# Kernel optimization log

Hardware: AMD Instinct MI355X
Metric: run time of the kernel (lower is better)

The kernel has to match this reference:

```python
import jax, jax.numpy as jnp
import numpy as np

WIN = 16; DIM = 256; HEADS = 8; B = 2; H = 256; W_ = 256
SEL = 0.25; TEMP = 1.0


def _conv(x, w, b, stride=1, pad=1, groups=1):
    y = jax.lax.conv_general_dilated(
        x, w, (stride, stride), [(pad, pad), (pad, pad)],
        dimension_numbers=('NCHW', 'OIHW', 'NCHW'), feature_group_count=groups)
    return y + b[None, :, None, None]


def _rel_pos_index(w):
    coords = np.stack(np.meshgrid(np.arange(w), np.arange(w), indexing='ij'), 0).reshape(2, -1)
    rel = (coords[:, :, None] - coords[:, None, :]).transpose(1, 2, 0) + w - 1
    return jnp.asarray(rel[:, :, 0] * (2 * w - 1) + rel[:, :, 1])


def setup_inputs():
    key = jax.random.key(0)
    ks = jax.random.split(key, 10)
    C, w = DIM, WIN
    p = lambda k, shp, s=0.02: jax.random.normal(k, shp, jnp.float32) * s
    return dict(
        x=jax.random.normal(ks[0], (B, H, W_, C), jnp.float32),
        sd_w1=p(ks[1], (4, C, 3, 3)), sd_b1=jnp.zeros((4,), jnp.float32),
        sd_w2=p(ks[2], (4, 4, w, w)), sd_b2=jnp.zeros((4,), jnp.float32),
        sd_w3=p(ks[3], (4, 4, 3, 3)), sd_b3=jnp.zeros((4,), jnp.float32),
        in_w=p(ks[4], (3 * C, C)), in_b=jnp.zeros((3 * C,), jnp.float32),
        pe_table=p(ks[5], ((2 * w - 1) ** 2, HEADS)),
        out_w=p(ks[6], (C, C)), out_b=jnp.zeros((C,), jnp.float32),
        oc_w=p(ks[7], (C, 1, 3, 3)), oc_b=jnp.zeros((C,), jnp.float32),
    )


def reference(x, sd_w1, sd_b1, sd_w2, sd_b2, sd_w3, sd_b3, in_w, in_b, pe_table, out_w, out_b, oc_w, oc_b):
    w = WIN; C = DIM; nH = HEADS; hd = C // nH
    xc = jnp.transpose(x, (0, 3, 1, 2))  # [B,C,H,W]
    Bn, _, Hh, Ww = xc.shape
    # --- sparse discriminator: per-window scores / gates / offsets ---
    sd = jax.nn.silu(_conv(xc, sd_w1, sd_b1))
    sd = jax.nn.silu(_conv(sd, sd_w2, sd_b2, stride=w, pad=0))
    sd = _conv(sd, sd_w3, sd_b3)                      # [B,4,Hw,Ww]
    scores = sd[:, 0]
    gates = jax.nn.sigmoid(sd[:, 1])
    offsets = jax.nn.sigmoid(sd[:, 2:4])
    Hw, Www = scores.shape[1], scores.shape[2]
    k = int(Hw * Www * SEL)
    # --- top-k window selection (eval: softmax, straight-through to 1) ---
    gs = jax.nn.softmax(scores.reshape(Bn, -1) / TEMP, axis=-1)
    vals, topk = jax.lax.top_k(gs, k)                 # [B,k]
    scores_delta = (jax.lax.stop_gradient(1.0 - vals) + vals).reshape(-1)
    h_idx = (topk // Www).reshape(-1)
    w_idx = (topk % Www).reshape(-1)
    b_idx = jnp.broadcast_to(jnp.arange(Bn)[:, None], (Bn, k)).reshape(-1)
    g = gates[b_idx, h_idx, w_idx]
    hard = (g > 0.5).astype(jnp.float32)
    gates_delta = jax.lax.stop_gradient(hard - g) + g
    # --- learned-offset window coordinates (trunc like .long()) ---
    h_off = (offsets[b_idx, 0, h_idx, w_idx] * w - w / 2.0).astype(jnp.int32)
    w_off = (offsets[b_idx, 1, h_idx, w_idx] * w - w / 2.0).astype(jnp.int32)
    h1 = jnp.clip(h_idx * w + h_off, 0, Hh - w)
    w1 = jnp.clip(w_idx * w + w_off, 0, Ww - w)
    # --- roi_align (aligned=False, 1 sample/bin): bilinear at half-pixel centers ---
    ar = jnp.arange(w, dtype=jnp.float32) + 0.5
    yy = jnp.clip(h1[:, None].astype(jnp.float32) + ar, 0.0, Hh - 1.0)  # [N,w]
    xx = jnp.clip(w1[:, None].astype(jnp.float32) + ar, 0.0, Ww - 1.0)
    y0 = jnp.floor(yy).astype(jnp.int32); ly = yy - y0
    x0 = jnp.floor(xx).astype(jnp.int32); lx = xx - x0
    y1p = jnp.minimum(y0 + 1, Hh - 1); x1p = jnp.minimum(x0 + 1, Ww - 1)
    bI = b_idx[:, None, None]
    gather = lambda ys, xs: xc[bI, :, ys[:, :, None], xs[:, None, :]]  # [N,w,w,C]
    wy1 = ly[:, :, None, None]; wy0 = 1.0 - wy1
    wx1 = lx[:, None, :, None]; wx0 = 1.0 - wx1
    x_before = (wy0 * wx0 * gather(y0, x0) + wy0 * wx1 * gather(y0, x1p)
                + wy1 * wx0 * gather(y1p, x0) + wy1 * wx1 * gather(y1p, x1p))
    N = x_before.shape[0]
    # --- windowed MHA with relative position bias ---
    qkv = x_before.reshape(N, w * w, C) @ in_w.T + in_b
    q, kk, v = jnp.split(qkv, 3, axis=-1)
    heads = lambda t: t.reshape(N, w * w, nH, hd).transpose(0, 2, 1, 3)
    q, kk, v = heads(q), heads(kk), heads(v)
    pe = pe_table[_rel_pos_index(w)].transpose(2, 0, 1)[None]  # [1,nH,w2,w2]
    attn = jax.nn.softmax(jnp.einsum('nhqd,nhkd->nhqk', q, kk) * hd ** (-0.5) + pe, axis=-1)
    o = jnp.einsum('nhqk,nhkd->nhqd', attn, v).transpose(0, 2, 1, 3).reshape(N, w, w, C)
    x_after = o @ out_w.T + out_b
    delta = (x_after - x_before) * (gates_delta * scores_delta)[:, None, None, None]
    delta = delta * hard[:, None, None, None]  # gate-dropped windows contribute nothing
    # --- scatter-reduce 'mean' back into the image ---
    abs_h = h1[:, None] + jnp.arange(w)
    abs_w = w1[:, None] + jnp.arange(w)
    flat = ((b_idx[:, None, None] * Hh + abs_h[:, :, None]) * Ww + abs_w[:, None, :]).reshape(-1)
    sums = jnp.zeros((Bn * Hh * Ww, C), jnp.float32).at[flat].add(delta.reshape(-1, C))
    cnts = jnp.zeros((Bn * Hh * Ww,), jnp.float32).at[flat].add(
        jnp.broadcast_to(hard[:, None, None], (N, w, w)).reshape(-1))
    mean = jnp.where(cnts[:, None] > 0, sums / jnp.maximum(cnts[:, None], 1.0), 0.0)
    xc = xc + mean.reshape(Bn, Hh, Ww, C).transpose(0, 3, 1, 2)
    out = _conv(xc, oc_w, oc_b, groups=C)  # depthwise 3x3
    return jnp.transpose(out, (0, 2, 3, 1))
```

## Files before the change

### kernel.cpp

```cpp
#include <hip/hip_runtime.h>

typedef __attribute__((ext_vector_type(8))) short short8v;
typedef __attribute__((ext_vector_type(4))) float f32x4;

#define DEV __device__ __forceinline__

DEV float sigmoidf_(float x){ return 1.0f/(1.0f+expf(-x)); }
DEV float siluf_(float x){ return x/(1.0f+expf(-x)); }
DEV ushort f2bf(float f){
  union{float f; unsigned u;} a; a.f = f;
  unsigned r = a.u + 0x7fffu + ((a.u >> 16) & 1u);
  return (ushort)(r >> 16);
}


__global__ void k_w36(const float* __restrict__ w1, float* __restrict__ w36){
  int i = blockIdx.x*256 + threadIdx.x;
  if (i < 9216){
    int kk = i % 9, o = (i/9) & 3, c = i / 36;
    w36[i] = w1[(o*256 + c)*9 + kk];
  }
}

__global__ __launch_bounds__(256) void k_c1a(const float* __restrict__ x,
    const float* __restrict__ w36, float* __restrict__ p36){
  int t = threadIdx.x;
  int p0 = blockIdx.x*512 + t;
  const float* xr0 = x + (size_t)p0*256;
  const float* xr1 = xr0 + 65536;
  float acc0[36], acc1[36];
  #pragma unroll
  for (int j=0;j<36;++j){ acc0[j]=0.f; acc1[j]=0.f; }
  for (int c4=0; c4<64; ++c4){
    float4 xv0 = *(const float4*)(xr0 + c4*4);
    float4 xv1 = *(const float4*)(xr1 + c4*4);
    float xs0[4] = {xv0.x, xv0.y, xv0.z, xv0.w};
    float xs1[4] = {xv1.x, xv1.y, xv1.z, xv1.w};
    #pragma unroll
    for (int e=0;e<4;++e){
      const float4* wrow = (const float4*)(w36 + (size_t)(c4*4+e)*36);
      float xe0 = xs0[e], xe1 = xs1[e];
      #pragma unroll
      for (int jv=0;jv<9;++jv){
        float4 wv = wrow[jv];
        acc0[jv*4+0] += xe0*wv.x; acc0[jv*4+1] += xe0*wv.y;
        acc0[jv*4+2] += xe0*wv.z; acc0[jv*4+3] += xe0*wv.w;
        acc1[jv*4+0] += xe1*wv.x; acc1[jv*4+1] += xe1*wv.y;
        acc1[jv*4+2] += xe1*wv.z; acc1[jv*4+3] += xe1*wv.w;
      }
    }
  }
  #pragma unroll
  for (int j=0;j<36;++j){
    p36[(size_t)j*131072 + p0]       = acc0[j];
    p36[(size_t)j*131072 + p0 + 256] = acc1[j];
  }
}

__global__ __launch_bounds__(256) void k_c1b(const float* __restrict__ p36,
    const float* __restrict__ b1, float* __restrict__ t1){
  int pix = blockIdx.x*256 + threadIdx.x;
  int xp = pix & 255, y = (pix>>8)&255, b = pix>>16;
  float a[4] = {b1[0], b1[1], b1[2], b1[3]};
  #pragma unroll
  for (int ky=0;ky<3;++ky){
    int yy = y+ky-1; if ((unsigned)yy>=256u) continue;
    #pragma unroll
    for (int kx=0;kx<3;++kx){
      int xx = xp+kx-1; if ((unsigned)xx>=256u) continue;
      int np = (b<<16) + yy*256 + xx;
      #pragma unroll
      for (int o=0;o<4;++o)
        a[o] += p36[(size_t)(o*9+ky*3+kx)*131072 + np];
    }
  }
  int base = b*262144 + y*256 + xp;
  t1[base]        = siluf_(a[0]);
  t1[base+65536]  = siluf_(a[1]);
  t1[base+131072] = siluf_(a[2]);
  t1[base+196608] = siluf_(a[3]);
}

__global__ void k_wq(const float* __restrict__ w, ushort* __restrict__ Wq, int nfrag){
  int i = blockIdx.x*256 + threadIdx.x;
  if (i >= nfrag) return;
  int l  = i & 63;
  int kc = (i >> 6) & 7;
  int jt = i >> 9;
  int j = jt*16 + (l & 15);
  int k = kc*32 + (l >> 4)*8;
  const float4* src = (const float4*)(w + j*256 + k);
  float4 v0 = src[0], v1 = src[1];
  union{ uint4 q; ushort u[8]; } o;
  o.u[0]=f2bf(v0.x); o.u[1]=f2bf(v0.y); o.u[2]=f2bf(v0.z); o.u[3]=f2bf(v0.w);
  o.u[4]=f2bf(v1.x); o.u[5]=f2bf(v1.y); o.u[6]=f2bf(v1.z); o.u[7]=f2bf(v1.w);
  *(uint4*)(Wq + (size_t)i*8) = o.q;
}

__global__ void k_conv2(const float* __restrict__ t1, const float* __restrict__ w2,
                        const float* __restrict__ b2, float* __restrict__ t2){
  int oidx = blockIdx.x;
  int ox = oidx & 15, oy = (oidx>>4)&15, o = (oidx>>8)&3, b = oidx>>10;
  int t = threadIdx.x;
  float acc = 0.f;
  #pragma unroll
  for (int uu=0; uu<4; ++uu){
    int u = t + uu*256;
    int ic = u >> 8, ky = (u>>4)&15, kx = u&15;
    float xv = t1[(b*4+ic)*65536 + (oy*16+ky)*256 + (ox*16+kx)];
    float wv = w2[(o*4+ic)*256 + ky*16 + kx];
    acc += xv*wv;
  }
  __shared__ float red[256];
  red[t] = acc; __syncthreads();
  for (int s=128; s>0; s>>=1){ if (t<s) red[t]+=red[t+s]; __syncthreads(); }
  if (t==0) t2[oidx] = siluf_(red[0] + b2[o]);
}

__global__ void k_conv3(const float* __restrict__ t2, const float* __restrict__ w3,
                        const float* __restrict__ b3, float* __restrict__ sd3){
  int i = blockIdx.x*256 + threadIdx.x;
  int ox = i & 15, oy = (i>>4)&15, o = (i>>8)&3, b = i>>10;
  float acc = b3[o];
  for (int ic=0; ic<4; ++ic){
    const float* src = t2 + (b*4+ic)*256;
    const float* ww  = w3 + (o*4+ic)*9;
    #pragma unroll
    for (int ky=0; ky<3; ++ky){
      int yy = oy + ky - 1; if ((unsigned)yy >= 16u) continue;
      #pragma unroll
      for (int kx=0; kx<3; ++kx){
        int xx = ox + kx - 1; if ((unsigned)xx >= 16u) continue;
        acc += src[yy*16+xx] * ww[ky*3+kx];
      }
    }
  }
  sd3[i] = acc;
}

__global__ void k_topk(const float* __restrict__ sd3, int* __restrict__ desc){
  int b = blockIdx.x, t = threadIdx.x;
  __shared__ float sc[256];
  sc[t] = sd3[(b*4+0)*256 + t];
  __syncthreads();
  float st = sc[t];
  int rank = 0;
  for (int j=0;j<256;++j){
    float sj = sc[j];
    rank += (sj > st) || (sj == st && j < t);
  }
  if (rank < 64){
    float g = sigmoidf_(sd3[(b*4+1)*256 + t]);
    int hard = (g > 0.5f) ? 1 : 0;
    float offh = sigmoidf_(sd3[(b*4+2)*256 + t]) * 16.0f - 8.0f;
    float offw = sigmoidf_(sd3[(b*4+3)*256 + t]) * 16.0f - 8.0f;
    int hoff = (int)offh, woff = (int)offw;
    int h1 = min(max((t>>4)*16 + hoff, 0), 240);
    int w1 = min(max((t&15)*16 + woff, 0), 240);
    ((int4*)desc)[b*64 + rank] = make_int4(h1, w1, hard, 0);
  }
}

__global__ __launch_bounds__(256) void k_xb(const float* __restrict__ x,
    const int* __restrict__ desc, float* __restrict__ XB){
  int wi = blockIdx.x;
  int4 d = ((const int4*)desc)[wi];
  if (!d.z) return;
  int b = wi >> 6;
  int ty = blockIdx.y;
  int tid = threadIdx.x;
  int tx = tid >> 4;
  int cl = (tid & 15) * 4;
  float yyf = fminf((float)(d.x + ty) + 0.5f, 255.0f);
  int y0 = (int)yyf; float ly = yyf - (float)y0; int y1 = min(y0+1, 255);
  float xxf = fminf((float)(d.y + tx) + 0.5f, 255.0f);
  int x0 = (int)xxf; float lx = xxf - (float)x0; int x1 = min(x0+1, 255);
  float w00=(1.f-ly)*(1.f-lx), w01=(1.f-ly)*lx, w10=ly*(1.f-lx), w11=ly*lx;
  const float* p00 = x + ((b*256+y0)*256 + x0)*256;
  const float* p01 = x + ((b*256+y0)*256 + x1)*256;
  const float* p10 = x + ((b*256+y1)*256 + x0)*256;
  const float* p11 = x + ((b*256+y1)*256 + x1)*256;
  float* dst = XB + (wi*256 + ty*16 + tx)*256;
  #pragma unroll
  for (int u=0; u<4; ++u){
    int c = cl + u*64;
    float4 A = *(const float4*)(p00+c);
    float4 Bv= *(const float4*)(p01+c);
    float4 Cv= *(const float4*)(p10+c);
    float4 Dv= *(const float4*)(p11+c);
    float4 r;
    r.x = w00*A.x + w01*Bv.x + w10*Cv.x + w11*Dv.x;
    r.y = w00*A.y + w01*Bv.y + w10*Cv.y + w11*Dv.y;
    r.z = w00*A.z + w01*Bv.z + w10*Cv.z + w11*Dv.z;
    r.w = w00*A.w + w01*Bv.w + w10*Cv.w + w11*Dv.w;
    *(float4*)(dst + c) = r;
  }
}

__global__ __launch_bounds__(256) void k_qkv(const float* __restrict__ XB,
    const ushort* __restrict__ Wq, const float* __restrict__ in_b,
    const int* __restrict__ desc, ushort* __restrict__ Qs,
    ushort* __restrict__ Kb, ushort* __restrict__ Vb){
  int wi = blockIdx.x;
  if (((const int4*)desc)[wi].z == 0) return;
  int t0 = blockIdx.y * 32;
  __shared__ __align__(16) ushort Xs[32*264];
  int tid = threadIdx.x;
  const float* Ab = XB + (size_t)(wi*256 + t0)*256;
  for (int i = tid; i < 2048; i += 256){
    int row = i >> 6, kq = (i & 63) * 4;
    float4 v = *(const float4*)(Ab + row*256 + kq);
    ushort4 u = make_ushort4(f2bf(v.x), f2bf(v.y), f2bf(v.z), f2bf(v.w));
    *(ushort4*)(&Xs[row*264 + kq]) = u;
  }
  __syncthreads();
  int w = tid >> 6, l = tid & 63;
  int lr = l & 15, lg = l >> 4;
  f32x4 acc[2][12];
  #pragma unroll
  for (int a=0;a<2;++a)
    #pragma unroll
    for (int j=0;j<12;++j) acc[a][j] = (f32x4){0.f,0.f,0.f,0.f};
  for (int kc = 0; kc < 8; ++kc){
    short8v xf0 = *(const short8v*)(&Xs[lr*264       + kc*32 + lg*8]);
    short8v xf1 = *(const short8v*)(&Xs[(16+lr)*264 + kc*32 + lg*8]);
    #pragma unroll
    for (int jt = 0; jt < 12; ++jt){
      short8v wf = *(const short8v*)(Wq + ((size_t)((w*12 + jt)*8 + kc)*64 + l)*8);
      acc[0][jt] = __builtin_amdgcn_mfma_f32_16x16x32_bf16(xf0, wf, acc[0][jt], 0, 0, 0);
      acc[1][jt] = __builtin_amdgcn_mfma_f32_16x16x32_bf16(xf1, wf, acc[1][jt], 0, 0, 0);
    }
  }
  #pragma unroll
  for (int ts=0; ts<2; ++ts)
    #pragma unroll
    for (int jt=0; jt<12; ++jt){
      int j = w*192 + jt*16 + lr;
      #pragma unroll
      for (int r=0; r<4; ++r){
        int t = t0 + ts*16 + lg*4 + r;
        float val = acc[ts][jt][r] + in_b[j];
        if (j < 256){
          Qs[((size_t)(wi*256 + t))*256 + j] = f2bf(val * 0.17677669529663687f);
        } else if (j < 512){
          int jq = j - 256;
          Kb[((size_t)(wi*8 + (jq>>5))*256 + t)*32 + (jq&31)] = f2bf(val);
        } else {
          int jq = j - 512;
          Vb[((size_t)(wi*8 + (jq>>5))*256 + t)*32 + (jq&31)] = f2bf(val);
        }
      }
    }
}

__global__ void k_pe(const float* __restrict__ pe_table, float* __restrict__ PEf){
  int id = blockIdx.x*256 + threadIdx.x;
  int h = id >> 16, q = (id>>8)&255, j = id&255;
  int ih = (q>>4) - (j>>4) + 15;
  int iw = (q&15) - (j&15) + 15;
  PEf[id] = pe_table[(ih*31+iw)*8 + h];
}

__global__ __launch_bounds__(256,2) void k_attn(const ushort* __restrict__ Qs,
    const ushort* __restrict__ Kb, const ushort* __restrict__ Vb,
    const float* __restrict__ PEf, const int* __restrict__ desc,
    ushort* __restrict__ Ob){
  int wi = blockIdx.x, h = blockIdx.y;
  if (((const int4*)desc)[wi].z == 0) return;
  __shared__ __align__(16) ushort Ks[256*40];
  __shared__ __align__(16) ushort Vt[32*264];
  __shared__ __align__(16) ushort Pb[4][16*40];
  int tid = threadIdx.x;
  {
    const uint4* src = (const uint4*)(Kb + (size_t)((wi*8+h)*256 + tid)*32);
    uint4 a = src[0], b = src[1], c = src[2], d = src[3];
    *(uint4*)(&Ks[tid*40 +  0]) = a;
    *(uint4*)(&Ks[tid*40 +  8]) = b;
    *(uint4*)(&Ks[tid*40 + 16]) = c;
    *(uint4*)(&Ks[tid*40 + 24]) = d;
  }
  {
    const uint4* src = (const uint4*)(Vb + (size_t)((wi*8+h)*256 + tid)*32);
    #pragma unroll
    for (int c4=0; c4<4; ++c4){
      union{uint4 v; ushort u[8];} uu; uu.v = src[c4];
      #pragma unroll
      for (int e=0;e<8;++e) Vt[(c4*8+e)*264 + tid] = uu.u[e];
    }
  }
  __syncthreads();
  int w = tid >> 6, l = tid & 63;
  int lg = l >> 4, lr = l & 15;
  const float* PEh = PEf + h*65536;
  for (int s_i = 0; s_i < 4; ++s_i){
    int q0 = (w*4 + s_i)*16;
    short8v qf = *(const short8v*)(Qs + ((size_t)(wi*256 + q0 + lr))*256 + h*32 + lg*8);
    f32x4 sfr[16];
    #pragma unroll
    for (int jt=0; jt<16; ++jt){
      f32x4 c;
      #pragma unroll
      for (int r=0;r<4;++r) c[r] = PEh[(q0 + lg*4 + r)*256 + jt*16 + lr];
      short8v kf = *(const short8v*)(&Ks[(jt*16 + lr)*40 + lg*8]);
      sfr[jt] = __builtin_amdgcn_mfma_f32_16x16x32_bf16(qf, kf, c, 0, 0, 0);
    }
    float mx[4] = {-1e30f,-1e30f,-1e30f,-1e30f};
    #pragma unroll
    for (int jt=0;jt<16;++jt)
      #pragma unroll
      for (int r=0;r<4;++r) mx[r] = fmaxf(mx[r], sfr[jt][r]);
    #pragma unroll
    for (int m_=1; m_<16; m_<<=1){
      #pragma unroll
      for (int r=0;r<4;++r) mx[r] = fmaxf(mx[r], __shfl_xor(mx[r], m_));
    }
    float sm[4] = {0.f,0.f,0.f,0.f};
    #pragma unroll
    for (int jt=0;jt<16;++jt)
      #pragma unroll
      for (int r=0;r<4;++r){
        float p = __expf(sfr[jt][r] - mx[r]);
        sfr[jt][r] = p; sm[r] += p;
      }
    #pragma unroll
    for (int m_=1; m_<16; m_<<=1){
      #pragma unroll
      for (int r=0;r<4;++r) sm[r] += __shfl_xor(sm[r], m_);
    }
    f32x4 oa0 = {0.f,0.f,0.f,0.f}, oa1 = {0.f,0.f,0.f,0.f};
    ushort* pb = Pb[w];
    #pragma unroll
    for (int kc=0; kc<8; ++kc){
      #pragma unroll
      for (int t2=0;t2<2;++t2)
        #pragma unroll
        for (int r=0;r<4;++r)
          pb[(lg*4+r)*40 + t2*16 + lr] = f2bf(sfr[kc*2+t2][r]);
      short8v pf = *(const short8v*)(&pb[lr*40 + lg*8]);
      short8v v0 = *(const short8v*)(&Vt[lr*264 + kc*32 + lg*8]);
      short8v v1 = *(const short8v*)(&Vt[(16+lr)*264 + kc*32 + lg*8]);
      oa0 = __builtin_amdgcn_mfma_f32_16x16x32_bf16(pf, v0, oa0, 0, 0, 0);
      oa1 = __builtin_amdgcn_mfma_f32_16x16x32_bf16(pf, v1, oa1, 0, 0, 0);
    }
    #pragma unroll
    for (int r=0;r<4;++r){
      float inv = 1.0f / sm[r];
      size_t obase = ((size_t)(wi*256 + q0 + lg*4 + r))*256 + h*32;
      Ob[obase + lr]      = f2bf(oa0[r] * inv);
      Ob[obase + 16 + lr] = f2bf(oa1[r] * inv);
    }
  }
}

__global__ void k_zero(const int* __restrict__ desc, float* __restrict__ sums,
                       float* __restrict__ cnts){
  int wi = blockIdx.x;
  int4 d = ((const int4*)desc)[wi];
  if (!d.z) return;
  int b = wi >> 6;
  int t = threadIdx.x;
  int pix = (b*256 + d.x + (t>>4))*256 + d.y + (t&15);
  float4* p = (float4*)(sums + (size_t)pix*256);
  #pragma unroll 8
  for (int c=0;c<64;++c) p[c] = make_float4(0.f,0.f,0.f,0.f);
  atomicAdd(&cnts[pix], 1.0f);
}

__global__ __launch_bounds__(256) void k_oproj(const ushort* __restrict__ Ob,
    const ushort* __restrict__ Wq2, const float* __restrict__ out_b,
    const float* __restrict__ XB, const int* __restrict__ desc,
    float* __restrict__ sums){
  int wi = blockIdx.x;
  int4 dsc = ((const int4*)desc)[wi];
  if (!dsc.z) return;
  int t0 = blockIdx.y * 32;
  __shared__ __align__(16) ushort Os[32*264];
  int tid = threadIdx.x;
  for (int i = tid; i < 1024; i += 256){
    int row = i >> 5, k8 = (i & 31) * 8;
    uint4 vv = *(const uint4*)(Ob + (size_t)(wi*256 + t0 + row)*256 + k8);
    *(uint4*)(&Os[row*264 + k8]) = vv;
  }
  __syncthreads();
  int w = tid >> 6, l = tid & 63;
  int lr = l & 15, lg = l >> 4;
  f32x4 acc[2][4];
  #pragma unroll
  for (int a=0;a<2;++a)
    #pragma unroll
    for (int j=0;j<4;++j) acc[a][j] = (f32x4){0.f,0.f,0.f,0.f};
  for (int kc = 0; kc < 8; ++kc){
    short8v of0 = *(const short8v*)(&Os[lr*264       + kc*32 + lg*8]);
    short8v of1 = *(const short8v*)(&Os[(16+lr)*264 + kc*32 + lg*8]);
    #pragma unroll
    for (int jt = 0; jt < 4; ++jt){
      short8v wf = *(const short8v*)(Wq2 + ((size_t)((w*4 + jt)*8 + kc)*64 + l)*8);
      acc[0][jt] = __builtin_amdgcn_mfma_f32_16x16x32_bf16(of0, wf, acc[0][jt], 0, 0, 0);
      acc[1][jt] = __builtin_amdgcn_mfma_f32_16x16x32_bf16(of1, wf, acc[1][jt], 0, 0, 0);
    }
  }
  int b = wi >> 6;
  #pragma unroll
  for (int ts=0; ts<2; ++ts)
    #pragma unroll
    for (int jt=0; jt<4; ++jt){
      int j = w*64 + jt*16 + lr;
      #pragma unroll
      for (int r=0; r<4; ++r){
        int t = t0 + ts*16 + lg*4 + r;
        int pix = (b*256 + dsc.x + (t>>4))*256 + dsc.y + (t&15);
        float delta = acc[ts][jt][r] + out_b[j] - XB[((size_t)(wi*256 + t))*256 + j];
        atomicAdd(&sums[(size_t)pix*256 + j], delta);
      }
    }
}

__global__ __launch_bounds__(256) void k_final(const float* __restrict__ x,
    const float* __restrict__ sums, const float* __restrict__ cnts,
    const float* __restrict__ ocw, const float* __restrict__ ocb,
    float* __restrict__ out){
  int x0 = blockIdx.x * 16;
  int y  = blockIdx.y;
  int b  = blockIdx.z;
  int c  = threadIdx.x;
  __shared__ float wl[2304];
  __shared__ float bl[256];
  __shared__ float invc[54];
  for (int i = threadIdx.x; i < 2304; i += 256) wl[i] = ocw[i];
  bl[c] = ocb[c];
  if (threadIdx.x < 54){
    int rr = threadIdx.x / 18, cc = threadIdx.x % 18;
    int yy = y + rr - 1, xx = x0 + cc - 1;
    float iv = 0.f;
    if ((unsigned)yy < 256u && (unsigned)xx < 256u){
      float cv = cnts[(b*256+yy)*256 + xx];
      if (cv > 0.f) iv = 1.0f / cv;
    }
    invc[threadIdx.x] = iv;
  }
  float v[3][18];
  #pragma unroll
  for (int rr=0; rr<3; ++rr){
    int yy = y + rr - 1;
    bool yok = (unsigned)yy < 256u;
    #pragma unroll
    for (int cc=0; cc<18; ++cc){
      int xx = x0 + cc - 1;
      v[rr][cc] = (yok && (unsigned)xx < 256u)
        ? x[((size_t)((b*256+yy)*256 + xx))*256 + c] : 0.f;
    }
  }
  __syncthreads();
  #pragma unroll
  for (int rr=0; rr<3; ++rr){
    int yy = y + rr - 1;
    #pragma unroll
    for (int cc=0; cc<18; ++cc){
      float iv = invc[rr*18 + cc];
      if (iv != 0.f){
        int xx = x0 + cc - 1;
        v[rr][cc] += sums[((size_t)((b*256+yy)*256 + xx))*256 + c] * iv;
      }
    }
  }
  float w0=wl[c*9+0], w1=wl[c*9+1], w2=wl[c*9+2],
        w3=wl[c*9+3], w4=wl[c*9+4], w5=wl[c*9+5],
        w6=wl[c*9+6], w7=wl[c*9+7], w8=wl[c*9+8];
  float bias = bl[c];
  size_t obase = ((size_t)((b*256+y)*256 + x0))*256 + c;
  #pragma unroll
  for (int oc=0; oc<16; ++oc){
    float acc = bias
      + w0*v[0][oc] + w1*v[0][oc+1] + w2*v[0][oc+2]
      + w3*v[1][oc] + w4*v[1][oc+1] + w5*v[1][oc+2]
      + w6*v[2][oc] + w7*v[2][oc+1] + w8*v[2][oc+2];
    out[obase + (size_t)oc*256] = acc;
  }
}

extern "C" void kernel_launch(void* const* d_in, const int* in_sizes, int n_in,
                              void* d_out, int out_size, void* d_ws, size_t ws_size,
                              hipStream_t stream){
  const float* x     = (const float*)d_in[0];
  const float* sd_w1 = (const float*)d_in[1];
  const float* sd_b1 = (const float*)d_in[2];
  const float* sd_w2 = (const float*)d_in[3];
  const float* sd_b2 = (const float*)d_in[4];
  const float* sd_w3 = (const float*)d_in[5];
  const float* sd_b3 = (const float*)d_in[6];
  const float* in_w  = (const float*)d_in[7];
  const float* in_b  = (const float*)d_in[8];
  const float* pe_t  = (const float*)d_in[9];
  const float* out_w = (const float*)d_in[10];
  const float* out_b = (const float*)d_in[11];
  const float* oc_w  = (const float*)d_in[12];
  const float* oc_b  = (const float*)d_in[13];
  float* out = (float*)d_out;
  char* ws = (char*)d_ws;
  if (ws_size < 204003328ULL) return;

  float*  w36 = (float*)(ws + 0);
  float*  t1  = (float*)(ws + 36864);
  float*  t2  = (float*)(ws + 2134016);
  float*  sd3 = (float*)(ws + 2142208);
  int*    desc= (int*)  (ws + 2150400);
  ushort* Wq  = (ushort*)(ws + 2152448);
  ushort* Wq2 = (ushort*)(ws + 2545664);
  float*  XB  = (float*)(ws + 2676736);
  float*  p36 = (float*)(ws + 2676736);
  ushort* Ob  = (ushort*)(ws + 36231168);
  float*  sums= (float*)(ws + 69261312);
  ushort* Qs  = (ushort*)(ws + 69261312);
  ushort* Kb  = (ushort*)(ws + 86038528);
  ushort* Vb  = (ushort*)(ws + 102815744);
  float*  PEf = (float*)(ws + 119592960);
  float*  cnts= (float*)(ws + 203479040);

  k_w36  <<<36,   256, 0, stream>>>(sd_w1, w36);
  k_wq   <<<96,   256, 0, stream>>>(in_w,  Wq,  24576);
  k_wq   <<<32,   256, 0, stream>>>(out_w, Wq2, 8192);
  k_c1a  <<<256,  256, 0, stream>>>(x, w36, p36);
  k_c1b  <<<512,  256, 0, stream>>>(p36, sd_b1, t1);
  k_conv2<<<2048, 256, 0, stream>>>(t1, sd_w2, sd_b2, t2);
  k_conv3<<<8,    256, 0, stream>>>(t2, sd_w3, sd_b3, sd3);
  k_topk <<<2,    256, 0, stream>>>(sd3, desc);
  k_pe   <<<2048, 256, 0, stream>>>(pe_t, PEf);
  k_xb   <<<dim3(128,16), 256, 0, stream>>>(x, desc, XB);
  k_qkv  <<<dim3(128,8),  256, 0, stream>>>(XB, Wq, in_b, desc, Qs, Kb, Vb);
  k_attn <<<dim3(128,8),  256, 0, stream>>>(Qs, Kb, Vb, PEf, desc, Ob);
  hipMemsetAsync(cnts, 0, 524288, stream);
  k_zero <<<128,  256, 0, stream>>>(desc, sums, cnts);
  k_oproj<<<dim3(128,8),  256, 0, stream>>>(Ob, Wq2, out_b, XB, desc, sums);
  k_final<<<dim3(16,256,2),256, 0, stream>>>(x, sums, cnts, oc_w, oc_b, out);
}
```

Before: 310.8 us.

## Restructure first conv projection to stage input in shared memory and split channels

The per-pixel 256-to-36 channel projection now loads input rows into shared memory with coalesced float4 loads instead of each thread reading its own strided row. Each block handles 128 pixels, and two thread halves each cover half of the channels before a shared-memory reduction. The grid grows from 256 to 1024 blocks, which gives more parallelism and halves the accumulator registers per thread. The cost is extra barriers and a final LDS reduction step.

```diff
diff --git a/kernel.cpp b/kernel.cpp
--- a/kernel.cpp
+++ b/kernel.cpp
@@ -24,36 +24,45 @@
 
 __global__ __launch_bounds__(256) void k_c1a(const float* __restrict__ x,
     const float* __restrict__ w36, float* __restrict__ p36){
-  int t = threadIdx.x;
-  int p0 = blockIdx.x*512 + t;
-  const float* xr0 = x + (size_t)p0*256;
-  const float* xr1 = xr0 + 65536;
-  float acc0[36], acc1[36];
-  #pragma unroll
-  for (int j=0;j<36;++j){ acc0[j]=0.f; acc1[j]=0.f; }
-  for (int c4=0; c4<64; ++c4){
-    float4 xv0 = *(const float4*)(xr0 + c4*4);
-    float4 xv1 = *(const float4*)(xr1 + c4*4);
-    float xs0[4] = {xv0.x, xv0.y, xv0.z, xv0.w};
-    float xs1[4] = {xv1.x, xv1.y, xv1.z, xv1.w};
-    #pragma unroll
-    for (int e=0;e<4;++e){
-      const float4* wrow = (const float4*)(w36 + (size_t)(c4*4+e)*36);
-      float xe0 = xs0[e], xe1 = xs1[e];
+  __shared__ __align__(16) float Xs[10240];
+  int tid = threadIdx.x;
+  int p0 = blockIdx.x * 128;
+  int pix = tid & 127, half = tid >> 7;
+  float acc[36];
+  #pragma unroll
+  for (int j=0;j<36;++j) acc[j]=0.f;
+  for (int cc=0; cc<4; ++cc){
+    __syncthreads();
+    #pragma unroll
+    for (int i=tid; i<2048; i+=256){
+      int row = i >> 4, q = (i & 15)*4;
+      *(float4*)(&Xs[row*68 + q]) =
+        *(const float4*)(x + (size_t)(p0+row)*256 + cc*64 + q);
+    }
+    __syncthreads();
+    const float* xr = &Xs[pix*68 + half*32];
+    const float* wb = w36 + (cc*64 + half*32)*36;
+    #pragma unroll
+    for (int c=0;c<32;++c){
+      float xv = xr[c];
+      const float4* wrow = (const float4*)(wb + c*36);
       #pragma unroll
       for (int jv=0;jv<9;++jv){
         float4 wv = wrow[jv];
-        acc0[jv*4+0] += xe0*wv.x; acc0[jv*4+1] += xe0*wv.y;
-        acc0[jv*4+2] += xe0*wv.z; acc0[jv*4+3] += xe0*wv.w;
-        acc1[jv*4+0] += xe1*wv.x; acc1[jv*4+1] += xe1*wv.y;
-        acc1[jv*4+2] += xe1*wv.z; acc1[jv*4+3] += xe1*wv.w;
+        acc[jv*4+0] += xv*wv.x; acc[jv*4+1] += xv*wv.y;
+        acc[jv*4+2] += xv*wv.z; acc[jv*4+3] += xv*wv.w;
       }
     }
   }
-  #pragma unroll
-  for (int j=0;j<36;++j){
-    p36[(size_t)j*131072 + p0]       = acc0[j];
-    p36[(size_t)j*131072 + p0 + 256] = acc1[j];
+  __syncthreads();
+  #pragma unroll
+  for (int j=0;j<36;++j) Xs[(half*128 + pix)*40 + j] = acc[j];
+  __syncthreads();
+  #pragma unroll
+  for (int jj=0;jj<18;++jj){
+    int j = half*18 + jj;
+    float v = Xs[pix*40 + j] + Xs[(128+pix)*40 + j];
+    p36[(size_t)j*131072 + p0 + pix] = v;
   }
 }
 
@@ -519,7 +528,7 @@
   k_w36  <<<36,   256, 0, stream>>>(sd_w1, w36);
   k_wq   <<<96,   256, 0, stream>>>(in_w,  Wq,  24576);
   k_wq   <<<32,   256, 0, stream>>>(out_w, Wq2, 8192);
-  k_c1a  <<<256,  256, 0, stream>>>(x, w36, p36);
+  k_c1a  <<<1024, 256, 0, stream>>>(x, w36, p36);
   k_c1b  <<<512,  256, 0, stream>>>(p36, sd_b1, t1);
   k_conv2<<<2048, 256, 0, stream>>>(t1, sd_w2, sd_b2, t2);
   k_conv3<<<8,    256, 0, stream>>>(t2, sd_w3, sd_b3, sd3);
```

After: 390.7 us. +25.7%, slower.
